# Performance work log

Hardware: AMD Instinct MI355X
Metric: run time of the kernel (lower is better)

Reference implementation:

```python
import jax, jax.numpy as jnp
import numpy as np

B, N, DIM = 2, 2048, 1024
HEADS, DH, NUM_MEM = 8, 64, 4
EPS = 1e-5


def layer_norm(x, gamma):
    mu = x.mean(-1, keepdims=True)
    var = ((x - mu) ** 2).mean(-1, keepdims=True)
    return (x - mu) * jax.lax.rsqrt(var + EPS) * gamma


def setup_inputs() -> dict:
    key = jax.random.key(0)
    ks = jax.random.split(key, 7)
    x = jax.random.normal(ks[0], (B, N, DIM), jnp.float32)
    mask = jax.random.randint(ks[1], (B, N), 0, 2) > 0
    attn_bias = jax.random.normal(ks[2], (HEADS, N, N), jnp.float32) * 0.02
    gamma = jnp.ones((DIM,), jnp.float32)
    Wq = jax.random.normal(ks[3], (DIM, HEADS * DH), jnp.float32) * (DIM ** -0.5)
    Wkv = jax.random.normal(ks[4], (DIM, 2 * DH), jnp.float32) * (DIM ** -0.5)
    mem_kv = jax.random.normal(ks[5], (2, NUM_MEM, DH), jnp.float32)
    Wout = jax.random.normal(ks[6], (HEADS * DH, DIM), jnp.float32) * ((HEADS * DH) ** -0.5)
    return dict(x=x, attn_bias=attn_bias, gamma=gamma, Wq=Wq, Wkv=Wkv,
                mem_kv=mem_kv, Wout=Wout, mask=mask)


def reference(x, attn_bias, gamma, Wq, Wkv, mem_kv, Wout, mask):
    b, n, _ = x.shape
    # norm applied to query path only; kv comes from pre-norm x (self-attention)
    xn = layer_norm(x, gamma)
    q = (xn @ Wq).reshape(b, n, HEADS, DH).transpose(0, 2, 1, 3) * (DH ** -0.5)  # b h n d
    kv = x @ Wkv  # multi-query: single shared kv head
    k, v = kv[..., :DH], kv[..., DH:]
    mk = jnp.broadcast_to(mem_kv[0], (b, NUM_MEM, DH))
    mv = jnp.broadcast_to(mem_kv[1], (b, NUM_MEM, DH))
    k = jnp.concatenate([mk, k], axis=1)  # b (m+n) d
    v = jnp.concatenate([mv, v], axis=1)
    j = n + NUM_MEM
    bias = jnp.pad(attn_bias, ((0, 0), (0, 0), (NUM_MEM, 0)))  # zero bias on mem tokens
    maskp = jnp.pad(mask, ((0, 0), (NUM_MEM, 0)), constant_values=True)
    sim = jnp.einsum('bhid,bjd->bhij', q, k) + bias
    neg = -jnp.finfo(sim.dtype).max
    sim = jnp.where(maskp[:, None, None, :], sim, neg)
    causal = jnp.triu(jnp.ones((n, j), bool), k=NUM_MEM + 1)  # mem tokens always visible
    sim = jnp.where(causal, neg, sim)
    attn = jax.nn.softmax(sim, axis=-1)
    out = jnp.einsum('bhij,bjd->bhid', attn, v)
    out = out.transpose(0, 2, 1, 3).reshape(b, n, HEADS * DH)
    return out @ Wout
```

## Files before the change

kernel.cpp:

```cpp
#include <hip/hip_runtime.h>
#include <hip/hip_bf16.h>
#include <float.h>

#define B_ 2
#define N_ 2048
#define DIM_ 1024
#define HEADS_ 8
#define DH_ 64
#define NUM_MEM_ 4
#define ROWS_ (B_ * N_)
#define QCOLS_ (HEADS_ * DH_)
#define JTOT_ (N_ + NUM_MEM_)
#define JPAD_ 2176
#define KPAD_ 72
#define CHUNKS_PER_BH_ 77

typedef __attribute__((ext_vector_type(8))) short short8v;
typedef __attribute__((ext_vector_type(4))) float f32x4;

static __device__ __forceinline__ ushort f2b(float f) {
    __hip_bfloat16 hb = __float2bfloat16(f);
    return *(ushort*)&hb;
}

__global__ __launch_bounds__(256) void ln_cast_kernel(const float* __restrict__ x,
                                                      const float* __restrict__ gamma,
                                                      ushort* __restrict__ xb,
                                                      ushort* __restrict__ xnb) {
    int row = blockIdx.x;
    const float4 v = ((const float4*)(x + (size_t)row * DIM_))[threadIdx.x];
    float s  = v.x + v.y + v.z + v.w;
    float s2 = v.x * v.x + v.y * v.y + v.z * v.z + v.w * v.w;
    #pragma unroll
    for (int off = 32; off > 0; off >>= 1) {
        s  += __shfl_down(s, off);
        s2 += __shfl_down(s2, off);
    }
    __shared__ float ws1[4], ws2[4];
    int lane = threadIdx.x & 63, wid = threadIdx.x >> 6;
    if (lane == 0) { ws1[wid] = s; ws2[wid] = s2; }
    __syncthreads();
    float tot  = ws1[0] + ws1[1] + ws1[2] + ws1[3];
    float tot2 = ws2[0] + ws2[1] + ws2[2] + ws2[3];
    float mu  = tot * (1.0f / DIM_);
    float var = tot2 * (1.0f / DIM_) - mu * mu;
    float rs  = rsqrtf(var + 1e-5f);
    const float4 g = ((const float4*)gamma)[threadIdx.x];
    float vv[4] = {v.x, v.y, v.z, v.w};
    float gg[4] = {g.x, g.y, g.z, g.w};
    ushort xo[4], xno[4];
    #pragma unroll
    for (int j = 0; j < 4; ++j) {
        xo[j]  = f2b(vv[j]);
        xno[j] = f2b((vv[j] - mu) * rs * gg[j]);
    }
    *(int2*)(xb  + (size_t)row * DIM_ + threadIdx.x * 4) = *(int2*)xo;
    *(int2*)(xnb + (size_t)row * DIM_ + threadIdx.x * 4) = *(int2*)xno;
}

static __device__ __forceinline__ void wtrans_body(const float* __restrict__ W,
                                                   ushort* __restrict__ Wt,
                                                   int K, int N, int t) {
    int n = t % N;
    int k0 = (t / N) * 8;
    ushort u[8];
    #pragma unroll
    for (int j = 0; j < 8; ++j) u[j] = f2b(W[(size_t)(k0 + j) * N + n]);
    *(int4*)(Wt + (size_t)n * K + k0) = *(int4*)u;
}

__global__ __launch_bounds__(256) void prep_kernel(const float* __restrict__ Wq,
                                                   const float* __restrict__ Wkv,
                                                   const float* __restrict__ Wout,
                                                   const float* __restrict__ mem_kv,
                                                   ushort* __restrict__ Wqt,
                                                   ushort* __restrict__ Wkvt,
                                                   ushort* __restrict__ Woutt,
                                                   ushort* __restrict__ Kb,
                                                   ushort* __restrict__ Vt) {
    int bid = blockIdx.x;
    int tid = threadIdx.x;
    if (bid < 256) {
        wtrans_body(Wq, Wqt, DIM_, QCOLS_, bid * 256 + tid);
    } else if (bid < 320) {
        wtrans_body(Wkv, Wkvt, DIM_, 2 * DH_, (bid - 256) * 256 + tid);
    } else if (bid < 576) {
        wtrans_body(Wout, Woutt, QCOLS_, DIM_, (bid - 320) * 256 + tid);
    } else {
        int t = (bid - 576) * 256 + tid;
        int d  = t & 63;
        int ji = (t >> 6) & 127;
        int b  = t >> 13;
        int j  = (ji < NUM_MEM_) ? ji : (2048 + ji);
        float kv_ = 0.f, vv = 0.f;
        if (ji < NUM_MEM_) {
            kv_ = mem_kv[ji * DH_ + d];
            vv  = mem_kv[NUM_MEM_ * DH_ + ji * DH_ + d];
        }
        Kb[((size_t)(b * JPAD_) + j) * DH_ + d] = f2b(kv_);
        Vt[((size_t)(b * DH_) + d) * JPAD_ + j] = f2b(vv);
    }
}

template<int MODE, int BM>
__global__ __launch_bounds__(256) void gemm_bf16(const ushort* __restrict__ A,
                                                 const ushort* __restrict__ Bt,
                                                 void* __restrict__ C,
                                                 void* __restrict__ C2,
                                                 int M, int N, int K) {
    constexpr int RT = BM / 64;
    __shared__ ushort As[BM][40];
    __shared__ ushort Bs[64][40];
    int tid = threadIdx.x;
    int w = tid >> 6, l = tid & 63, lg = l >> 4, ll = l & 15;
    int r0 = blockIdx.y * BM, c0 = blockIdx.x * 64;

    int arow = tid >> 2;
    int achk = (tid & 3) * 8;
    const ushort* Ap  = A + (size_t)(r0 + arow) * K + achk;
    const ushort* Ap2 = Ap + (size_t)64 * K;
    const ushort* Bp  = Bt + (size_t)(c0 + arow) * K + achk;

    int4 a0 = *(const int4*)Ap;
    int4 a1;
    if constexpr (RT == 2) a1 = *(const int4*)Ap2;
    int4 b0 = *(const int4*)Bp;

    f32x4 acc[RT][4] = {};

    int nk = K / 32;
    for (int ks = 0; ks < nk; ++ks) {
        __syncthreads();
        *(int4*)&As[arow][achk] = a0;
        if constexpr (RT == 2) *(int4*)&As[arow + 64][achk] = a1;
        *(int4*)&Bs[arow][achk] = b0;
        __syncthreads();
        int kn = (ks + 1 < nk) ? (ks + 1) * 32 : 0;
        a0 = *(const int4*)(Ap + kn);
        if constexpr (RT == 2) a1 = *(const int4*)(Ap2 + kn);
        b0 = *(const int4*)(Bp + kn);
        short8v af[RT], bf[4];
        #pragma unroll
        for (int rt = 0; rt < RT; ++rt)
            af[rt] = *(const short8v*)&As[w * 16 * RT + rt * 16 + ll][lg * 8];
        #pragma unroll
        for (int ct = 0; ct < 4; ++ct)
            bf[ct] = *(const short8v*)&Bs[ct * 16 + ll][lg * 8];
        __builtin_amdgcn_s_setprio(1);
        #pragma unroll
        for (int rt = 0; rt < RT; ++rt)
            #pragma unroll
            for (int ct = 0; ct < 4; ++ct)
                acc[rt][ct] = __builtin_amdgcn_mfma_f32_16x16x32_bf16(af[rt], bf[ct], acc[rt][ct], 0, 0, 0);
        __builtin_amdgcn_s_setprio(0);
    }

    #pragma unroll
    for (int rt = 0; rt < RT; ++rt) {
        #pragma unroll
        for (int ct = 0; ct < 4; ++ct) {
            #pragma unroll
            for (int r = 0; r < 4; ++r) {
                int row = r0 + w * 16 * RT + rt * 16 + lg * 4 + r;
                int col = c0 + ct * 16 + ll;
                float val = acc[rt][ct][r];
                if (MODE == 0) {
                    ((ushort*)C)[(size_t)row * QCOLS_ + col] = f2b(val * 0.125f);
                } else if (MODE == 1) {
                    int b = row >> 11;
                    int j = (row & 2047) + NUM_MEM_;
                    if (col < DH_)
                        ((ushort*)C)[((size_t)(b * JPAD_) + j) * DH_ + col] = f2b(val);
                    else
                        ((ushort*)C2)[((size_t)(b * DH_) + (col - DH_)) * JPAD_ + j] = f2b(val);
                } else {
                    ((float*)C)[(size_t)row * DIM_ + col] = val;
                }
            }
        }
    }
}

__global__ __launch_bounds__(256) void fattn_split_kernel(const ushort* __restrict__ qb,
                                                          const ushort* __restrict__ Kb,
                                                          const ushort* __restrict__ Vt,
                                                          const float* __restrict__ bias,
                                                          const int* __restrict__ mask,
                                                          float* __restrict__ part_O,
                                                          float* __restrict__ part_ml) {
    __shared__ ushort Ks[64][KPAD_];
    __shared__ ushort Vs[64][KPAD_];
    __shared__ ushort Ps[4][16][KPAD_];

    int cid = blockIdx.x;
    int bh  = cid / CHUNKS_PER_BH_;
    int rem = cid - bh * CHUNKS_PER_BH_;
    int b = bh >> 3, h = bh & 7;
    int qt = 0, ci = 0;
    {
        int cum = 0;
        #pragma unroll 1
        for (int t = 0; t < 32; ++t) {
            int c = (t + 10) / 9;
            if (rem < cum + c) { qt = t; ci = rem - cum; break; }
            cum += c;
        }
    }
    int nt = qt + 2;
    int nc = (qt + 10) / 9;
    int t0 = ci * nt / nc;
    int t1 = (ci + 1) * nt / nc;
    int q0 = qt * 64;

    int tid = threadIdx.x;
    int w  = tid >> 6;
    int l  = tid & 63;
    int lg = l >> 4;
    int ll = l & 15;
    int i_base = q0 + w * 16;

    short8v aq0, aq1;
    {
        int i = i_base + ll;
        const ushort* qp = qb + ((size_t)(b * N_ + i)) * QCOLS_ + h * DH_;
        aq0 = *(const short8v*)(qp + lg * 8);
        aq1 = *(const short8v*)(qp + 32 + lg * 8);
    }

    const float* brow0 = bias + ((size_t)h * N_ + i_base + lg * 4 + 0) * N_;
    const float* brow1 = bias + ((size_t)h * N_ + i_base + lg * 4 + 1) * N_;
    const float* brow2 = bias + ((size_t)h * N_ + i_base + lg * 4 + 2) * N_;
    const float* brow3 = bias + ((size_t)h * N_ + i_base + lg * 4 + 3) * N_;
    const int* mrowp = mask + b * N_;

    int sr = tid >> 3, sc = (tid & 7) * 8;
    const ushort* KbB = Kb + (size_t)b * JPAD_ * DH_;
    const ushort* VtB = Vt + (size_t)b * DH_ * JPAD_;

    int jp0 = t0 * 64;
    int4 kr0 = *(const int4*)(KbB + (size_t)(jp0 + sr) * DH_ + sc);
    int4 kr1 = *(const int4*)(KbB + (size_t)(jp0 + sr + 32) * DH_ + sc);
    int4 vr0 = *(const int4*)(VtB + (size_t)sr * JPAD_ + jp0 + sc);
    int4 vr1 = *(const int4*)(VtB + (size_t)(sr + 32) * JPAD_ + jp0 + sc);
    float bbc[16];
    int   mkc[4];
    #pragma unroll
    for (int ct = 0; ct < 4; ++ct) {
        int jj = jp0 + ct * 16 + ll;
        int sj = jj - NUM_MEM_;
        sj = sj < 0 ? 0 : (sj > N_ - 1 ? N_ - 1 : sj);
        mkc[ct] = mrowp[sj];
        bbc[ct * 4 + 0] = brow0[sj];
        bbc[ct * 4 + 1] = brow1[sj];
        bbc[ct * 4 + 2] = brow2[sj];
        bbc[ct * 4 + 3] = brow3[sj];
    }

    f32x4 oacc[4] = {};
    float mrow[4], lsum[4];
    #pragma unroll
    for (int r = 0; r < 4; ++r) { mrow[r] = -1e30f; lsum[r] = 0.f; }

    for (int jt = t0; jt < t1; ++jt) {
        int j0 = jt * 64;
        __syncthreads();
        *(int4*)&Ks[sr][sc]      = kr0;
        *(int4*)&Ks[sr + 32][sc] = kr1;
        *(int4*)&Vs[sr][sc]      = vr0;
        *(int4*)&Vs[sr + 32][sc] = vr1;
        __syncthreads();

        int jn0 = (jt + 1 < t1 ? jt + 1 : jt) * 64;
        kr0 = *(const int4*)(KbB + (size_t)(jn0 + sr) * DH_ + sc);
        kr1 = *(const int4*)(KbB + (size_t)(jn0 + sr + 32) * DH_ + sc);
        vr0 = *(const int4*)(VtB + (size_t)sr * JPAD_ + jn0 + sc);
        vr1 = *(const int4*)(VtB + (size_t)(sr + 32) * JPAD_ + jn0 + sc);
        float bbn[16];
        int   mkn[4];
        #pragma unroll
        for (int ct = 0; ct < 4; ++ct) {
            int jj = jn0 + ct * 16 + ll;
            int sj = jj - NUM_MEM_;
            sj = sj < 0 ? 0 : (sj > N_ - 1 ? N_ - 1 : sj);
            mkn[ct] = mrowp[sj];
            bbn[ct * 4 + 0] = brow0[sj];
            bbn[ct * 4 + 1] = brow1[sj];
            bbn[ct * 4 + 2] = brow2[sj];
            bbn[ct * 4 + 3] = brow3[sj];
        }

        float sv[4][4];
        #pragma unroll
        for (int ct = 0; ct < 4; ++ct) {
            f32x4 acc = {};
            short8v bk0 = *(const short8v*)&Ks[ct * 16 + ll][lg * 8];
            short8v bk1 = *(const short8v*)&Ks[ct * 16 + ll][32 + lg * 8];
            __builtin_amdgcn_s_setprio(1);
            acc = __builtin_amdgcn_mfma_f32_16x16x32_bf16(aq0, bk0, acc, 0, 0, 0);
            acc = __builtin_amdgcn_mfma_f32_16x16x32_bf16(aq1, bk1, acc, 0, 0, 0);
            __builtin_amdgcn_s_setprio(0);
            int jj = j0 + ct * 16 + ll;
            #pragma unroll
            for (int r = 0; r < 4; ++r) {
                int i = i_base + lg * 4 + r;
                float withb = mkc[ct] ? acc[r] + bbc[ct * 4 + r] : -1e30f;
                float s = (jj < NUM_MEM_) ? acc[r] : withb;
                sv[ct][r] = (jj <= i + NUM_MEM_) ? s : -1e30f;
            }
        }

        float scale_[4];
        #pragma unroll
        for (int r = 0; r < 4; ++r) {
            float t = fmaxf(fmaxf(sv[0][r], sv[1][r]), fmaxf(sv[2][r], sv[3][r]));
            #pragma unroll
            for (int off = 1; off < 16; off <<= 1) t = fmaxf(t, __shfl_xor(t, off));
            float mn = fmaxf(mrow[r], t);
            scale_[r] = __expf(mrow[r] - mn);
            mrow[r] = mn;
        }
        float psum[4] = {0.f, 0.f, 0.f, 0.f};
        #pragma unroll
        for (int ct = 0; ct < 4; ++ct) {
            #pragma unroll
            for (int r = 0; r < 4; ++r) {
                float p = __expf(sv[ct][r] - mrow[r]);
                psum[r] += p;
                Ps[w][lg * 4 + r][ct * 16 + ll] = f2b(p);
            }
        }
        #pragma unroll
        for (int r = 0; r < 4; ++r) {
            float t = psum[r];
            #pragma unroll
            for (int off = 1; off < 16; off <<= 1) t += __shfl_xor(t, off);
            lsum[r] = lsum[r] * scale_[r] + t;
        }
        #pragma unroll
        for (int dt = 0; dt < 4; ++dt)
            #pragma unroll
            for (int r = 0; r < 4; ++r) oacc[dt][r] *= scale_[r];

        #pragma unroll
        for (int c = 0; c < 2; ++c) {
            short8v ap = *(const short8v*)&Ps[w][ll][c * 32 + lg * 8];
            __builtin_amdgcn_s_setprio(1);
            #pragma unroll
            for (int dt = 0; dt < 4; ++dt) {
                short8v bv = *(const short8v*)&Vs[dt * 16 + ll][c * 32 + lg * 8];
                oacc[dt] = __builtin_amdgcn_mfma_f32_16x16x32_bf16(ap, bv, oacc[dt], 0, 0, 0);
            }
            __builtin_amdgcn_s_setprio(0);
        }

        #pragma unroll
        for (int u = 0; u < 16; ++u) bbc[u] = bbn[u];
        #pragma unroll
        for (int u = 0; u < 4; ++u) mkc[u] = mkn[u];
    }

    int slot = (bh * 32 + qt) * 4 + ci;
    float* po = part_O + (size_t)slot * 4096;
    #pragma unroll
    for (int dt = 0; dt < 4; ++dt)
        #pragma unroll
        for (int r = 0; r < 4; ++r)
            po[(w * 16 + lg * 4 + r) * 64 + dt * 16 + ll] = oacc[dt][r];
    if (ll == 0) {
        #pragma unroll
        for (int r = 0; r < 4; ++r) {
            int row = w * 16 + lg * 4 + r;
            part_ml[(size_t)slot * 128 + row * 2]     = mrow[r];
            part_ml[(size_t)slot * 128 + row * 2 + 1] = lsum[r];
        }
    }
}

__global__ __launch_bounds__(256) void merge_kernel(const float* __restrict__ part_O,
                                                    const float* __restrict__ part_ml,
                                                    ushort* __restrict__ attn_ob) {
    int bid = blockIdx.x;
    int qt = bid & 31;
    int bh = bid >> 5;
    int b = bh >> 3, h = bh & 7;
    int nc = (qt + 10) / 9;
    int tid = threadIdx.x;
    int row = tid >> 2;
    int dseg = (tid & 3) * 16;
    int slot0 = bid * 4;

    float M = -1e30f;
    #pragma unroll
    for (int c = 0; c < 4; ++c) {
        if (c >= nc) break;
        M = fmaxf(M, part_ml[(size_t)(slot0 + c) * 128 + row * 2]);
    }
    float den = 0.f;
    float num[16] = {};
    #pragma unroll
    for (int c = 0; c < 4; ++c) {
        if (c >= nc) break;
        float m_c = part_ml[(size_t)(slot0 + c) * 128 + row * 2];
        float l_c = part_ml[(size_t)(slot0 + c) * 128 + row * 2 + 1];
        float wgt = __expf(m_c - M);
        den += wgt * l_c;
        const float4* src = (const float4*)(part_O + (size_t)(slot0 + c) * 4096 + row * 64 + dseg);
        #pragma unroll
        for (int e = 0; e < 4; ++e) {
            float4 v = src[e];
            num[e * 4 + 0] += wgt * v.x;
            num[e * 4 + 1] += wgt * v.y;
            num[e * 4 + 2] += wgt * v.z;
            num[e * 4 + 3] += wgt * v.w;
        }
    }
    float inv = 1.f / den;
    ushort o[16];
    #pragma unroll
    for (int e = 0; e < 16; ++e) o[e] = f2b(num[e] * inv);
    int i = qt * 64 + row;
    ushort* dst = attn_ob + ((size_t)(b * N_ + i)) * QCOLS_ + h * DH_ + dseg;
    *(int4*)dst = *(int4*)o;
    *(int4*)(dst + 8) = *(int4*)(o + 8);
}

extern "C" void kernel_launch(void* const* d_in, const int* in_sizes, int n_in,
                              void* d_out, int out_size, void* d_ws, size_t ws_size,
                              hipStream_t stream) {
    const float* x         = (const float*)d_in[0];
    const float* attn_bias = (const float*)d_in[1];
    const float* gamma     = (const float*)d_in[2];
    const float* Wq        = (const float*)d_in[3];
    const float* Wkv       = (const float*)d_in[4];
    const float* mem_kv    = (const float*)d_in[5];
    const float* Wout      = (const float*)d_in[6];
    const int*   mask      = (const int*)d_in[7];
    float* out = (float*)d_out;

    char* wsb = (char*)d_ws;
    ushort* xb      = (ushort*)wsb;
    ushort* xnb     = (ushort*)(wsb + (8u  << 20));
    ushort* qb      = (ushort*)(wsb + (16u << 20));
    ushort* attn_ob = (ushort*)(wsb + (20u << 20));
    ushort* Kb      = (ushort*)(wsb + (24u << 20));
    ushort* Vt      = (ushort*)(wsb + (25u << 20));
    ushort* Wqt     = (ushort*)(wsb + (26u << 20));
    ushort* Wkvt    = (ushort*)(wsb + (27u << 20));
    ushort* Woutt   = (ushort*)(wsb + (28u << 20));
    float*  part_O  = (float*)(wsb + (32u << 20));
    float*  part_ml = (float*)(wsb + (64u << 20));

    ln_cast_kernel<<<ROWS_, 256, 0, stream>>>(x, gamma, xb, xnb);
    prep_kernel<<<640, 256, 0, stream>>>(Wq, Wkv, Wout, mem_kv, Wqt, Wkvt, Woutt, Kb, Vt);

    gemm_bf16<0, 64><<<dim3(QCOLS_ / 64, ROWS_ / 64), 256, 0, stream>>>(xnb, Wqt, qb, nullptr, ROWS_, QCOLS_, DIM_);
    gemm_bf16<1, 64><<<dim3((2 * DH_) / 64, ROWS_ / 64), 256, 0, stream>>>(xb, Wkvt, Kb, Vt, ROWS_, 2 * DH_, DIM_);
    fattn_split_kernel<<<16 * CHUNKS_PER_BH_, 256, 0, stream>>>(qb, Kb, Vt, attn_bias, mask, part_O, part_ml);
    merge_kernel<<<512, 256, 0, stream>>>(part_O, part_ml, attn_ob);
    gemm_bf16<2, 128><<<dim3(DIM_ / 64, ROWS_ / 128), 256, 0, stream>>>(attn_ob, Woutt, out, nullptr, ROWS_, DIM_, QCOLS_);
}
```

Measured before the change: 115.9 us.

## Transpose attention MFMA tiles and stage packed bf16 bias/mask through LDS

Swaps the MFMA operand order so each lane owns a single query row, which cuts the row max and sum reductions to two cross-group shuffles and one running max/sum per lane, and allows vectorized f32x4 output stores. Bias, mask and causal masking are now loaded coalesced as float2 per thread, folded into one packed bf16 value and staged in LDS, replacing the scattered per-lane scalar bias loads. The P tile is written with packed uint2 stores. The cost is an extra LDS buffer and a bf16 rounding of the bias, which slightly changes numerics.

```diff
diff --git a/kernel.cpp b/kernel.cpp
--- a/kernel.cpp
+++ b/kernel.cpp
@@ -12,7 +12,6 @@
 #define QCOLS_ (HEADS_ * DH_)
 #define JTOT_ (N_ + NUM_MEM_)
 #define JPAD_ 2176
-#define KPAD_ 72
 #define CHUNKS_PER_BH_ 77
 
 typedef __attribute__((ext_vector_type(8))) short short8v;
@@ -21,6 +20,15 @@
 static __device__ __forceinline__ ushort f2b(float f) {
     __hip_bfloat16 hb = __float2bfloat16(f);
     return *(ushort*)&hb;
+}
+static __device__ __forceinline__ uint pk2(float a, float b) {
+    return ((uint)f2b(b) << 16) | (uint)f2b(a);
+}
+static __device__ __forceinline__ float b2f_lo(uint u) {
+    union { uint x; float f; } c; c.x = u << 16; return c.f;
+}
+static __device__ __forceinline__ float b2f_hi(uint u) {
+    union { uint x; float f; } c; c.x = u & 0xffff0000u; return c.f;
 }
 
 __global__ __launch_bounds__(256) void ln_cast_kernel(const float* __restrict__ x,
@@ -188,9 +196,10 @@
                                                           const int* __restrict__ mask,
                                                           float* __restrict__ part_O,
                                                           float* __restrict__ part_ml) {
-    __shared__ ushort Ks[64][KPAD_];
-    __shared__ ushort Vs[64][KPAD_];
-    __shared__ ushort Ps[4][16][KPAD_];
+    __shared__ ushort Ks[64][72];
+    __shared__ ushort Vs[64][72];
+    __shared__ ushort Pt[4][16][72];
+    __shared__ ushort Bb[64][68];
 
     int cid = blockIdx.x;
     int bh  = cid / CHUNKS_PER_BH_;
@@ -217,57 +226,64 @@
     int l  = tid & 63;
     int lg = l >> 4;
     int ll = l & 15;
-    int i_base = q0 + w * 16;
+    int i_row = q0 + w * 16 + ll;
 
     short8v aq0, aq1;
     {
-        int i = i_base + ll;
-        const ushort* qp = qb + ((size_t)(b * N_ + i)) * QCOLS_ + h * DH_;
+        const ushort* qp = qb + ((size_t)(b * N_ + i_row)) * QCOLS_ + h * DH_;
         aq0 = *(const short8v*)(qp + lg * 8);
         aq1 = *(const short8v*)(qp + 32 + lg * 8);
     }
 
-    const float* brow0 = bias + ((size_t)h * N_ + i_base + lg * 4 + 0) * N_;
-    const float* brow1 = bias + ((size_t)h * N_ + i_base + lg * 4 + 1) * N_;
-    const float* brow2 = bias + ((size_t)h * N_ + i_base + lg * 4 + 2) * N_;
-    const float* brow3 = bias + ((size_t)h * N_ + i_base + lg * 4 + 3) * N_;
+    int trow = tid >> 5;
+    int tpc  = tid & 31;
+    const float* bias_rb = bias + ((size_t)h * N_ + q0 + trow) * N_;
     const int* mrowp = mask + b * N_;
 
     int sr = tid >> 3, sc = (tid & 7) * 8;
     const ushort* KbB = Kb + (size_t)b * JPAD_ * DH_;
     const ushort* VtB = Vt + (size_t)b * DH_ * JPAD_;
+
+    auto stage_bias = [&](int j0, uint* bbx) {
+        int j_e = j0 + 2 * tpc;
+        int sj  = j_e - NUM_MEM_;
+        int sjc = sj < 0 ? 0 : (sj > N_ - 2 ? N_ - 2 : sj);
+        int2 mk2 = *(const int2*)(mrowp + sjc);
+        float2 bv[8];
+        #pragma unroll
+        for (int p = 0; p < 8; ++p)
+            bv[p] = *(const float2*)(bias_rb + (size_t)(8 * p) * N_ + sjc);
+        #pragma unroll
+        for (int p = 0; p < 8; ++p) {
+            int i_s = q0 + trow + 8 * p;
+            float v0 = (j_e     < NUM_MEM_) ? 0.f : (mk2.x ? bv[p].x : -1e30f);
+            float v1 = (j_e + 1 < NUM_MEM_) ? 0.f : (mk2.y ? bv[p].y : -1e30f);
+            v0 = (j_e     <= i_s + NUM_MEM_) ? v0 : -1e30f;
+            v1 = (j_e + 1 <= i_s + NUM_MEM_) ? v1 : -1e30f;
+            bbx[p] = pk2(v0, v1);
+        }
+    };
 
     int jp0 = t0 * 64;
     int4 kr0 = *(const int4*)(KbB + (size_t)(jp0 + sr) * DH_ + sc);
     int4 kr1 = *(const int4*)(KbB + (size_t)(jp0 + sr + 32) * DH_ + sc);
     int4 vr0 = *(const int4*)(VtB + (size_t)sr * JPAD_ + jp0 + sc);
     int4 vr1 = *(const int4*)(VtB + (size_t)(sr + 32) * JPAD_ + jp0 + sc);
-    float bbc[16];
-    int   mkc[4];
-    #pragma unroll
-    for (int ct = 0; ct < 4; ++ct) {
-        int jj = jp0 + ct * 16 + ll;
-        int sj = jj - NUM_MEM_;
-        sj = sj < 0 ? 0 : (sj > N_ - 1 ? N_ - 1 : sj);
-        mkc[ct] = mrowp[sj];
-        bbc[ct * 4 + 0] = brow0[sj];
-        bbc[ct * 4 + 1] = brow1[sj];
-        bbc[ct * 4 + 2] = brow2[sj];
-        bbc[ct * 4 + 3] = brow3[sj];
-    }
+    uint bbc[8], bbn[8];
+    stage_bias(jp0, bbc);
 
     f32x4 oacc[4] = {};
-    float mrow[4], lsum[4];
-    #pragma unroll
-    for (int r = 0; r < 4; ++r) { mrow[r] = -1e30f; lsum[r] = 0.f; }
+    float mrow1 = -1e30f, lsum1 = 0.f;
 
     for (int jt = t0; jt < t1; ++jt) {
-        int j0 = jt * 64;
         __syncthreads();
         *(int4*)&Ks[sr][sc]      = kr0;
         *(int4*)&Ks[sr + 32][sc] = kr1;
         *(int4*)&Vs[sr][sc]      = vr0;
         *(int4*)&Vs[sr + 32][sc] = vr1;
+        #pragma unroll
+        for (int p = 0; p < 8; ++p)
+            *(uint*)&Bb[trow + 8 * p][2 * tpc] = bbc[p];
         __syncthreads();
 
         int jn0 = (jt + 1 < t1 ? jt + 1 : jt) * 64;
@@ -275,104 +291,85 @@
         kr1 = *(const int4*)(KbB + (size_t)(jn0 + sr + 32) * DH_ + sc);
         vr0 = *(const int4*)(VtB + (size_t)sr * JPAD_ + jn0 + sc);
         vr1 = *(const int4*)(VtB + (size_t)(sr + 32) * JPAD_ + jn0 + sc);
-        float bbn[16];
-        int   mkn[4];
-        #pragma unroll
-        for (int ct = 0; ct < 4; ++ct) {
-            int jj = jn0 + ct * 16 + ll;
-            int sj = jj - NUM_MEM_;
-            sj = sj < 0 ? 0 : (sj > N_ - 1 ? N_ - 1 : sj);
-            mkn[ct] = mrowp[sj];
-            bbn[ct * 4 + 0] = brow0[sj];
-            bbn[ct * 4 + 1] = brow1[sj];
-            bbn[ct * 4 + 2] = brow2[sj];
-            bbn[ct * 4 + 3] = brow3[sj];
-        }
-
-        float sv[4][4];
+        stage_bias(jn0, bbn);
+
+        float s[4][4];
         #pragma unroll
         for (int ct = 0; ct < 4; ++ct) {
             f32x4 acc = {};
             short8v bk0 = *(const short8v*)&Ks[ct * 16 + ll][lg * 8];
             short8v bk1 = *(const short8v*)&Ks[ct * 16 + ll][32 + lg * 8];
             __builtin_amdgcn_s_setprio(1);
-            acc = __builtin_amdgcn_mfma_f32_16x16x32_bf16(aq0, bk0, acc, 0, 0, 0);
-            acc = __builtin_amdgcn_mfma_f32_16x16x32_bf16(aq1, bk1, acc, 0, 0, 0);
+            acc = __builtin_amdgcn_mfma_f32_16x16x32_bf16(bk0, aq0, acc, 0, 0, 0);
+            acc = __builtin_amdgcn_mfma_f32_16x16x32_bf16(bk1, aq1, acc, 0, 0, 0);
             __builtin_amdgcn_s_setprio(0);
-            int jj = j0 + ct * 16 + ll;
+            uint2 ub = *(const uint2*)&Bb[w * 16 + ll][ct * 16 + lg * 4];
+            s[ct][0] = acc[0] + b2f_lo(ub.x);
+            s[ct][1] = acc[1] + b2f_hi(ub.x);
+            s[ct][2] = acc[2] + b2f_lo(ub.y);
+            s[ct][3] = acc[3] + b2f_hi(ub.y);
+        }
+
+        float m01 = fmaxf(fmaxf(s[0][0], s[0][1]), fmaxf(s[0][2], s[0][3]));
+        float m23 = fmaxf(fmaxf(s[1][0], s[1][1]), fmaxf(s[1][2], s[1][3]));
+        float m45 = fmaxf(fmaxf(s[2][0], s[2][1]), fmaxf(s[2][2], s[2][3]));
+        float m67 = fmaxf(fmaxf(s[3][0], s[3][1]), fmaxf(s[3][2], s[3][3]));
+        float m = fmaxf(fmaxf(m01, m23), fmaxf(m45, m67));
+        m = fmaxf(m, __shfl_xor(m, 16));
+        m = fmaxf(m, __shfl_xor(m, 32));
+        float mn = fmaxf(mrow1, m);
+        float scl = __expf(mrow1 - mn);
+        mrow1 = mn;
+
+        float ps = 0.f;
+        #pragma unroll
+        for (int ct = 0; ct < 4; ++ct)
             #pragma unroll
             for (int r = 0; r < 4; ++r) {
-                int i = i_base + lg * 4 + r;
-                float withb = mkc[ct] ? acc[r] + bbc[ct * 4 + r] : -1e30f;
-                float s = (jj < NUM_MEM_) ? acc[r] : withb;
-                sv[ct][r] = (jj <= i + NUM_MEM_) ? s : -1e30f;
+                float p = __expf(s[ct][r] - mn);
+                s[ct][r] = p;
+                ps += p;
             }
-        }
-
-        float scale_[4];
-        #pragma unroll
-        for (int r = 0; r < 4; ++r) {
-            float t = fmaxf(fmaxf(sv[0][r], sv[1][r]), fmaxf(sv[2][r], sv[3][r]));
-            #pragma unroll
-            for (int off = 1; off < 16; off <<= 1) t = fmaxf(t, __shfl_xor(t, off));
-            float mn = fmaxf(mrow[r], t);
-            scale_[r] = __expf(mrow[r] - mn);
-            mrow[r] = mn;
-        }
-        float psum[4] = {0.f, 0.f, 0.f, 0.f};
+        ps += __shfl_xor(ps, 16);
+        ps += __shfl_xor(ps, 32);
+        lsum1 = lsum1 * scl + ps;
+
         #pragma unroll
         for (int ct = 0; ct < 4; ++ct) {
-            #pragma unroll
-            for (int r = 0; r < 4; ++r) {
-                float p = __expf(sv[ct][r] - mrow[r]);
-                psum[r] += p;
-                Ps[w][lg * 4 + r][ct * 16 + ll] = f2b(p);
-            }
-        }
-        #pragma unroll
-        for (int r = 0; r < 4; ++r) {
-            float t = psum[r];
-            #pragma unroll
-            for (int off = 1; off < 16; off <<= 1) t += __shfl_xor(t, off);
-            lsum[r] = lsum[r] * scale_[r] + t;
+            uint2 pu;
+            pu.x = pk2(s[ct][0], s[ct][1]);
+            pu.y = pk2(s[ct][2], s[ct][3]);
+            *(uint2*)&Pt[w][ll][ct * 16 + lg * 4] = pu;
         }
         #pragma unroll
         for (int dt = 0; dt < 4; ++dt)
             #pragma unroll
-            for (int r = 0; r < 4; ++r) oacc[dt][r] *= scale_[r];
+            for (int r = 0; r < 4; ++r) oacc[dt][r] *= scl;
 
         #pragma unroll
         for (int c = 0; c < 2; ++c) {
-            short8v ap = *(const short8v*)&Ps[w][ll][c * 32 + lg * 8];
+            short8v ptf = *(const short8v*)&Pt[w][ll][c * 32 + lg * 8];
             __builtin_amdgcn_s_setprio(1);
             #pragma unroll
             for (int dt = 0; dt < 4; ++dt) {
                 short8v bv = *(const short8v*)&Vs[dt * 16 + ll][c * 32 + lg * 8];
-                oacc[dt] = __builtin_amdgcn_mfma_f32_16x16x32_bf16(ap, bv, oacc[dt], 0, 0, 0);
+                oacc[dt] = __builtin_amdgcn_mfma_f32_16x16x32_bf16(bv, ptf, oacc[dt], 0, 0, 0);
             }
             __builtin_amdgcn_s_setprio(0);
         }
 
         #pragma unroll
-        for (int u = 0; u < 16; ++u) bbc[u] = bbn[u];
-        #pragma unroll
-        for (int u = 0; u < 4; ++u) mkc[u] = mkn[u];
+        for (int u = 0; u < 8; ++u) bbc[u] = bbn[u];
     }
 
     int slot = (bh * 32 + qt) * 4 + ci;
     float* po = part_O + (size_t)slot * 4096;
     #pragma unroll
     for (int dt = 0; dt < 4; ++dt)
-        #pragma unroll
-        for (int r = 0; r < 4; ++r)
-            po[(w * 16 + lg * 4 + r) * 64 + dt * 16 + ll] = oacc[dt][r];
-    if (ll == 0) {
-        #pragma unroll
-        for (int r = 0; r < 4; ++r) {
-            int row = w * 16 + lg * 4 + r;
-            part_ml[(size_t)slot * 128 + row * 2]     = mrow[r];
-            part_ml[(size_t)slot * 128 + row * 2 + 1] = lsum[r];
-        }
+        *(f32x4*)&po[(w * 16 + ll) * 64 + dt * 16 + lg * 4] = oacc[dt];
+    if (lg == 0) {
+        part_ml[(size_t)slot * 128 + (w * 16 + ll) * 2]     = mrow1;
+        part_ml[(size_t)slot * 128 + (w * 16 + ll) * 2 + 1] = lsum1;
     }
 }
 
```

Result: faster. 110.5 us (-4.6%).
